# Kernel optimization log

Measured on AMD Instinct MI355X. Metric: run time of the kernel, lower is better.

Reference implementation:

```python
import jax, jax.numpy as jnp
import numpy as np

N_HEADS = 16
SEG_LEN = 512
MSG_LEN = 1536
T_TOTAL = SEG_LEN + MSG_LEN  # 2048


def _build_mask(T):
    # rows < SEG_LEN: attend to all cols < SEG_LEN (full, non-causal block)
    # rows >= SEG_LEN: standard causal (cols <= row)
    rows = jnp.arange(T)[:, None]
    cols = jnp.arange(T)[None, :]
    mask = jnp.where(rows < SEG_LEN, cols < SEG_LEN, cols <= rows)
    return mask  # [T, T] bool


def setup_inputs() -> dict:
    key = jax.random.key(0)
    k1, k2, k3 = jax.random.split(key, 3)
    B, T, E = 4, T_TOTAL, 1024
    x = jax.random.normal(k1, (B, T, E), dtype=jnp.float32)
    W_qkv = jax.random.normal(k2, (E, 3 * E), dtype=jnp.float32) * (1.0 / np.sqrt(E))
    b_qkv = jnp.zeros((3 * E,), dtype=jnp.float32)
    W_proj = jax.random.normal(k3, (E, E), dtype=jnp.float32) * (1.0 / np.sqrt(E))
    b_proj = jnp.zeros((E,), dtype=jnp.float32)
    return {"x": x, "W_qkv": W_qkv, "b_qkv": b_qkv, "W_proj": W_proj, "b_proj": b_proj}


def reference(x, W_qkv, b_qkv, W_proj, b_proj):
    B, T, E = x.shape
    H = N_HEADS
    D = E // H
    qkv = x @ W_qkv + b_qkv  # [B, T, 3E]
    q, k, v = jnp.split(qkv, 3, axis=-1)
    # [B, H, T, D]
    q = q.reshape(B, T, H, D).transpose(0, 2, 1, 3)
    k = k.reshape(B, T, H, D).transpose(0, 2, 1, 3)
    v = v.reshape(B, T, H, D).transpose(0, 2, 1, 3)
    att = jnp.einsum("bhqd,bhkd->bhqk", q, k) * (1.0 / np.sqrt(D))
    mask = _build_mask(T)  # [T, T]
    att = jnp.where(mask[None, None], att, jnp.float32(-jnp.inf))
    att = jax.nn.softmax(att, axis=-1)
    y = jnp.einsum("bhqk,bhkd->bhqd", att, v)
    y = y.transpose(0, 2, 1, 3).reshape(B, T, E)
    return y @ W_proj + b_proj
```

## Files before the change

### kernel.cpp

```cpp
#include <hip/hip_runtime.h>


typedef _Float16 f16;
typedef _Float16 f16x4 __attribute__((ext_vector_type(4)));
typedef _Float16 f16x8 __attribute__((ext_vector_type(8)));
typedef float f32x4 __attribute__((ext_vector_type(4)));

#define MFMA16x32(a, b, c) __builtin_amdgcn_mfma_f32_16x16x32_f16(a, b, c, 0, 0, 0)
#define MFMA16x16(a, b, c) __builtin_amdgcn_mfma_f32_16x16x16f16(a, b, c, 0, 0, 0)

__device__ __forceinline__ void gload_lds16(const void* g, void* l) {
  __builtin_amdgcn_global_load_lds(
      (__attribute__((address_space(1))) void*)g,
      (__attribute__((address_space(3))) void*)l, 16, 0, 0);
}


__global__ void k_cast_f16(const float* __restrict__ x, f16* __restrict__ xh) {
  int i = blockIdx.x * 256 + threadIdx.x;
  float4 v = ((const float4*)x)[i];
  f16x4 o = {(f16)v.x, (f16)v.y, (f16)v.z, (f16)v.w};
  ((f16x4*)xh)[i] = o;
}

__global__ void k_transpose(const float* __restrict__ W, f16* __restrict__ Wt,
                            int Kdim, int Ndim) {
  __shared__ float tile[32][33];
  int n = blockIdx.x * 32 + threadIdx.x;
  int k0 = blockIdx.y * 32;
  for (int j = threadIdx.y; j < 32; j += 8)
    tile[j][threadIdx.x] = W[(size_t)(k0 + j) * Ndim + n];
  __syncthreads();
  int k = k0 + threadIdx.x;
  for (int j = threadIdx.y; j < 32; j += 8)
    Wt[(size_t)(blockIdx.x * 32 + j) * Kdim + k] = (f16)tile[threadIdx.x][j];
}


__global__ __launch_bounds__(256) void k_gemm_qkv(
    const f16* __restrict__ A, const f16* __restrict__ Bt,
    const float* __restrict__ bias,
    f16* __restrict__ Qo, f16* __restrict__ Ko, f16* __restrict__ Vo) {
  constexpr int KD = 1024;
  __shared__ __align__(16) f16 As[128 * 32];
  __shared__ __align__(16) f16 Bs[128 * 32];
  __shared__ __align__(16) f16 Esh[4 * 64 * 72];
  const int tid = threadIdx.x;
  const int wave = tid >> 6, lane = tid & 63;
  const int g = lane >> 4, l16 = lane & 15;
  const int m0 = blockIdx.y * 128, n0 = blockIdx.x * 128;
  const int wm = (wave >> 1) * 64, wn = (wave & 1) * 64;
  const int srow = wave * 16 + (lane >> 2);
  const int skc = (lane & 3) * 8;

  f32x4 acc[4][4] = {};

  for (int k0 = 0; k0 < KD; k0 += 32) {
    __syncthreads();
    for (int it = 0; it < 2; ++it) {
      gload_lds16(A + (size_t)(m0 + it * 64 + srow) * KD + k0 + skc,
                  As + (it * 64 + wave * 16) * 32);
      gload_lds16(Bt + (size_t)(n0 + it * 64 + srow) * KD + k0 + skc,
                  Bs + (it * 64 + wave * 16) * 32);
    }
    __syncthreads();
    f16x8 af[4], bf[4];
    for (int mi = 0; mi < 4; ++mi)
      af[mi] = *(const f16x8*)(As + (wm + mi * 16 + l16) * 32 + g * 8);
    for (int ni = 0; ni < 4; ++ni)
      bf[ni] = *(const f16x8*)(Bs + (wn + ni * 16 + l16) * 32 + g * 8);
    for (int mi = 0; mi < 4; ++mi)
      for (int ni = 0; ni < 4; ++ni)
        acc[mi][ni] = MFMA16x32(af[mi], bf[ni], acc[mi][ni]);
  }

  const int nsub = n0 + wn;
  const int part = nsub >> 10;
  const int h    = (nsub >> 6) & 15;
  const int mg   = m0 + wm;
  const int b    = mg >> 11;
  const int tb   = mg & 2047;
  const size_t bh = (size_t)(b * 16 + h);
  f16* Es = Esh + wave * (64 * 72);

  float bv[4];
  for (int ni = 0; ni < 4; ++ni) bv[ni] = bias[nsub + ni * 16 + l16];

  for (int mi = 0; mi < 4; ++mi)
    for (int ni = 0; ni < 4; ++ni)
      for (int r = 0; r < 4; ++r) {
        f16 hv = (f16)(acc[mi][ni][r] + bv[ni]);
        int mrow = mi * 16 + g * 4 + r, ncol = ni * 16 + l16;
        if (part == 2) Es[ncol * 72 + mrow] = hv;
        else           Es[mrow * 72 + ncol] = hv;
      }

  const int rrow = lane >> 3, rcol = (lane & 7) * 8;
  for (int p = 0; p < 8; ++p) {
    int row = p * 8 + rrow;
    f16x8 vv = *(const f16x8*)(Es + row * 72 + rcol);
    if (part == 0)
      *(f16x8*)(Qo + (bh * 2048 + tb + row) * 64 + rcol) = vv;
    else if (part == 1)
      *(f16x8*)(Ko + (bh * 2048 + tb + row) * 64 + rcol) = vv;
    else
      *(f16x8*)(Vo + (bh * 64 + row) * 2048 + tb + rcol) = vv;
  }
}


__constant__ unsigned char cQA[10] = {15, 14, 13, 12, 11, 10, 9, 8, 7, 5};
__constant__ unsigned char cQB[10] = {255, 255, 255, 255, 0, 1, 2, 3, 6, 4};

__global__ __launch_bounds__(256, 4) void k_attn(
    const f16* __restrict__ Q, const f16* __restrict__ Kb,
    const f16* __restrict__ Vt, f16* __restrict__ Y) {
  __shared__ __align__(16) f16 Ks[64 * 64];
  __shared__ __align__(16) f16 Vs[64 * 64];
  __shared__ __align__(16) f16 Es[4 * 32 * 72];
  __shared__ float rs[4 * 32];

  const int tid = threadIdx.x;
  const int wave = tid >> 6, lane = tid & 63;
  const int g = lane >> 4, l16 = lane & 15;
  const int bh = blockIdx.y;
  const int b = bh >> 4, h = bh & 15;
  const int srowrel = lane >> 3;
  const int sc = (lane & 7) ^ srowrel;

  const f32x4 sinit = {-8.65617025f, -8.65617025f, -8.65617025f, -8.65617025f};

  for (int pass = 0; pass < 2; ++pass) {
    const int qt = pass ? (int)cQB[blockIdx.x] : (int)cQA[blockIdx.x];
    if (qt == 255) break;
    const int q0 = qt * 128;
    const int nt = (qt < 4) ? 8 : (qt + 1) * 2;

    f16x8 aq[2][2];
    for (int mi = 0; mi < 2; ++mi) {
      const f16* qrow =
          Q + ((size_t)bh * 2048 + q0 + wave * 32 + mi * 16 + l16) * 64 + g * 8;
      aq[mi][0] = *(const f16x8*)(qrow);
      aq[mi][1] = *(const f16x8*)(qrow + 32);
      for (int kb = 0; kb < 2; ++kb)
        aq[mi][kb] = aq[mi][kb] * (f16)0.18033688f;
    }

    f32x4 o[2][4] = {};
    float rsum[2] = {};

    for (int i = 0; i < nt; ++i) {
      const int kt0 = i << 6;
      __syncthreads();
      for (int it = 0; it < 2; ++it) {
        int row = it * 32 + wave * 8 + srowrel;
        gload_lds16(Kb + ((size_t)bh * 2048 + kt0 + row) * 64 + sc * 8,
                    Ks + (it * 32 + wave * 8) * 64);
        gload_lds16(Vt + ((size_t)bh * 64 + row) * 2048 + kt0 + sc * 8,
                    Vs + (it * 32 + wave * 8) * 64);
      }
      __syncthreads();

      f32x4 t[2][4];
      for (int nb = 0; nb < 4; ++nb) {
        int R = nb * 16 + l16, sw = R & 7;
        f16x8 bk0 = *(const f16x8*)(Ks + R * 64 + ((0 + g) ^ sw) * 8);
        f16x8 bk1 = *(const f16x8*)(Ks + R * 64 + ((4 + g) ^ sw) * 8);
        for (int mi = 0; mi < 2; ++mi) {
          f32x4 acc = MFMA16x32(bk0, aq[mi][0], sinit);
          t[mi][nb] = MFMA16x32(bk1, aq[mi][1], acc);
        }
      }

      const bool masked = (q0 >= 512) && (kt0 >= q0);
      f16x4 ap[4][2];
      for (int mi = 0; mi < 2; ++mi) {
        const int mrow = q0 + wave * 32 + mi * 16 + l16;
        for (int nb = 0; nb < 4; ++nb)
          for (int r = 0; r < 4; ++r) {
            float p = __builtin_amdgcn_exp2f(t[mi][nb][r]);
            if (masked && (kt0 + nb * 16 + g * 4 + r > mrow)) p = 0.f;
            rsum[mi] += p;
            ap[nb][mi][r] = (f16)p;
          }
      }

      for (int db = 0; db < 4; ++db)
        for (int nb = 0; nb < 4; ++nb) {
          int R = db * 16 + l16, sw = R & 7;
          int c = nb * 2 + (g >> 1);
          f16x4 bv = *(const f16x4*)(Vs + R * 64 + (c ^ sw) * 8 + (g & 1) * 4);
          for (int mi = 0; mi < 2; ++mi)
            o[mi][db] = MFMA16x16(ap[nb][mi], bv, o[mi][db]);
        }
    }

    for (int mi = 0; mi < 2; ++mi) {
      rsum[mi] += __shfl_xor(rsum[mi], 16, 64);
      rsum[mi] += __shfl_xor(rsum[mi], 32, 64);
    }

    if (g == 0)
      for (int mi = 0; mi < 2; ++mi) rs[wave * 32 + mi * 16 + l16] = rsum[mi];
    float rinv[2][4];
    for (int mi = 0; mi < 2; ++mi)
      for (int r = 0; r < 4; ++r)
        rinv[mi][r] = 1.0f / rs[wave * 32 + mi * 16 + g * 4 + r];

    f16* Ew = Es + wave * (32 * 72);
    for (int mi = 0; mi < 2; ++mi)
      for (int db = 0; db < 4; ++db)
        for (int r = 0; r < 4; ++r)
          Ew[(mi * 16 + g * 4 + r) * 72 + db * 16 + l16] =
              (f16)(o[mi][db][r] * rinv[mi][r]);

    const int rrow = lane >> 3, rcol = (lane & 7) * 8;
    const size_t ybase = (size_t)b * 2048 + q0 + wave * 32;
    for (int p = 0; p < 4; ++p) {
      int row = p * 8 + rrow;
      f16x8 vv = *(const f16x8*)(Ew + row * 72 + rcol);
      *(f16x8*)(Y + (ybase + row) * 1024 + h * 64 + rcol) = vv;
    }
  }
}


__global__ __launch_bounds__(256) void k_gemm_proj(
    const f16* __restrict__ A, const f16* __restrict__ Bt,
    const float* __restrict__ bias, float* __restrict__ out) {
  constexpr int KD = 1024;
  __shared__ __align__(16) f16 As[128 * 32];
  __shared__ __align__(16) f16 Bs[128 * 32];
  const int tid = threadIdx.x;
  const int wave = tid >> 6, lane = tid & 63;
  const int g = lane >> 4, l16 = lane & 15;
  const int m0 = blockIdx.y * 128, n0 = blockIdx.x * 128;
  const int wm = (wave >> 1) * 64, wn = (wave & 1) * 64;
  const int srow = wave * 16 + (lane >> 2);
  const int skc = (lane & 3) * 8;

  f32x4 acc[4][4] = {};

  for (int k0 = 0; k0 < KD; k0 += 32) {
    __syncthreads();
    for (int it = 0; it < 2; ++it) {
      gload_lds16(A + (size_t)(m0 + it * 64 + srow) * KD + k0 + skc,
                  As + (it * 64 + wave * 16) * 32);
      gload_lds16(Bt + (size_t)(n0 + it * 64 + srow) * KD + k0 + skc,
                  Bs + (it * 64 + wave * 16) * 32);
    }
    __syncthreads();
    f16x8 af[4], bf[4];
    for (int mi = 0; mi < 4; ++mi)
      af[mi] = *(const f16x8*)(As + (wm + mi * 16 + l16) * 32 + g * 8);
    for (int ni = 0; ni < 4; ++ni)
      bf[ni] = *(const f16x8*)(Bs + (wn + ni * 16 + l16) * 32 + g * 8);
    for (int mi = 0; mi < 4; ++mi)
      for (int ni = 0; ni < 4; ++ni)
        acc[mi][ni] = MFMA16x32(af[mi], bf[ni], acc[mi][ni]);
  }

  float bv[4];
  for (int ni = 0; ni < 4; ++ni) bv[ni] = bias[n0 + wn + ni * 16 + l16];

  for (int mi = 0; mi < 4; ++mi)
    for (int ni = 0; ni < 4; ++ni)
      for (int r = 0; r < 4; ++r) {
        int m = m0 + wm + mi * 16 + g * 4 + r;
        int n = n0 + wn + ni * 16 + l16;
        out[(size_t)m * 1024 + n] = acc[mi][ni][r] + bv[ni];
      }
}


extern "C" void kernel_launch(void* const* d_in, const int* in_sizes, int n_in,
                              void* d_out, int out_size, void* d_ws,
                              size_t ws_size, hipStream_t stream) {
  const float* x      = (const float*)d_in[0];
  const float* W_qkv  = (const float*)d_in[1];
  const float* b_qkv  = (const float*)d_in[2];
  const float* W_proj = (const float*)d_in[3];
  const float* b_proj = (const float*)d_in[4];
  float* out = (float*)d_out;

  char* ws = (char*)d_ws;
  f16* xh    = (f16*)ws;   ws += (size_t)8192 * 1024 * 2;
  f16* Wqt   = (f16*)ws;   ws += (size_t)3072 * 1024 * 2;
  f16* Wpt   = (f16*)ws;   ws += (size_t)1024 * 1024 * 2;
  f16* Qb    = (f16*)ws;   ws += (size_t)64 * 2048 * 64 * 2;
  f16* Kb    = (f16*)ws;   ws += (size_t)64 * 2048 * 64 * 2;
  f16* Vt    = (f16*)ws;   ws += (size_t)64 * 64 * 2048 * 2;
  f16* Y = xh;

  k_cast_f16<<<8192, 256, 0, stream>>>(x, xh);
  k_transpose<<<dim3(96, 32), dim3(32, 8), 0, stream>>>(W_qkv, Wqt, 1024, 3072);
  k_transpose<<<dim3(32, 32), dim3(32, 8), 0, stream>>>(W_proj, Wpt, 1024, 1024);
  k_gemm_qkv<<<dim3(24, 64), 256, 0, stream>>>(xh, Wqt, b_qkv, Qb, Kb, Vt);
  k_attn<<<dim3(10, 64), 256, 0, stream>>>(Qb, Kb, Vt, Y);
  k_gemm_proj<<<dim3(8, 64), 256, 0, stream>>>(Y, Wpt, b_proj, out);
}
```

Measured before the change: 287.1 us.

## Double-buffer K/V tiles in attention kernel to overlap loads with compute

```diff
diff --git a/kernel.cpp b/kernel.cpp
--- a/kernel.cpp
+++ b/kernel.cpp
@@ -112,11 +112,11 @@
 __constant__ unsigned char cQA[10] = {15, 14, 13, 12, 11, 10, 9, 8, 7, 5};
 __constant__ unsigned char cQB[10] = {255, 255, 255, 255, 0, 1, 2, 3, 6, 4};
 
-__global__ __launch_bounds__(256, 4) void k_attn(
+__global__ __launch_bounds__(256, 3) void k_attn(
     const f16* __restrict__ Q, const f16* __restrict__ Kb,
     const f16* __restrict__ Vt, f16* __restrict__ Y) {
-  __shared__ __align__(16) f16 Ks[64 * 64];
-  __shared__ __align__(16) f16 Vs[64 * 64];
+  __shared__ __align__(16) f16 Ks[2][64 * 64];
+  __shared__ __align__(16) f16 Vs[2][64 * 64];
   __shared__ __align__(16) f16 Es[4 * 32 * 72];
   __shared__ float rs[4 * 32];
 
@@ -127,6 +127,7 @@
   const int b = bh >> 4, h = bh & 15;
   const int srowrel = lane >> 3;
   const int sc = (lane & 7) ^ srowrel;
+  const int srw = wave * 8 + srowrel;
 
   const f32x4 sinit = {-8.65617025f, -8.65617025f, -8.65617025f, -8.65617025f};
 
@@ -149,23 +150,37 @@
     f32x4 o[2][4] = {};
     float rsum[2] = {};
 
+    for (int it = 0; it < 2; ++it) {
+      int row = it * 32 + srw;
+      gload_lds16(Kb + ((size_t)bh * 2048 + row) * 64 + sc * 8,
+                  &Ks[0][(it * 32 + wave * 8) * 64]);
+      gload_lds16(Vt + ((size_t)bh * 64 + row) * 2048 + sc * 8,
+                  &Vs[0][(it * 32 + wave * 8) * 64]);
+    }
+    __syncthreads();
+
+    int cur = 0;
     for (int i = 0; i < nt; ++i) {
+      if (i + 1 < nt) {
+        const int kn0 = (i + 1) << 6;
+        for (int it = 0; it < 2; ++it) {
+          int row = it * 32 + srw;
+          gload_lds16(Kb + ((size_t)bh * 2048 + kn0 + row) * 64 + sc * 8,
+                      &Ks[cur ^ 1][(it * 32 + wave * 8) * 64]);
+          gload_lds16(Vt + ((size_t)bh * 64 + row) * 2048 + kn0 + sc * 8,
+                      &Vs[cur ^ 1][(it * 32 + wave * 8) * 64]);
+        }
+      }
+
       const int kt0 = i << 6;
-      __syncthreads();
-      for (int it = 0; it < 2; ++it) {
-        int row = it * 32 + wave * 8 + srowrel;
-        gload_lds16(Kb + ((size_t)bh * 2048 + kt0 + row) * 64 + sc * 8,
-                    Ks + (it * 32 + wave * 8) * 64);
-        gload_lds16(Vt + ((size_t)bh * 64 + row) * 2048 + kt0 + sc * 8,
-                    Vs + (it * 32 + wave * 8) * 64);
-      }
-      __syncthreads();
+      const f16* Kc = Ks[cur];
+      const f16* Vc = Vs[cur];
 
       f32x4 t[2][4];
       for (int nb = 0; nb < 4; ++nb) {
         int R = nb * 16 + l16, sw = R & 7;
-        f16x8 bk0 = *(const f16x8*)(Ks + R * 64 + ((0 + g) ^ sw) * 8);
-        f16x8 bk1 = *(const f16x8*)(Ks + R * 64 + ((4 + g) ^ sw) * 8);
+        f16x8 bk0 = *(const f16x8*)(Kc + R * 64 + ((0 + g) ^ sw) * 8);
+        f16x8 bk1 = *(const f16x8*)(Kc + R * 64 + ((4 + g) ^ sw) * 8);
         for (int mi = 0; mi < 2; ++mi) {
           f32x4 acc = MFMA16x32(bk0, aq[mi][0], sinit);
           t[mi][nb] = MFMA16x32(bk1, aq[mi][1], acc);
@@ -189,10 +204,13 @@
         for (int nb = 0; nb < 4; ++nb) {
           int R = db * 16 + l16, sw = R & 7;
           int c = nb * 2 + (g >> 1);
-          f16x4 bv = *(const f16x4*)(Vs + R * 64 + (c ^ sw) * 8 + (g & 1) * 4);
+          f16x4 bv = *(const f16x4*)(Vc + R * 64 + (c ^ sw) * 8 + (g & 1) * 4);
           for (int mi = 0; mi < 2; ++mi)
             o[mi][db] = MFMA16x16(ap[nb][mi], bv, o[mi][db]);
         }
+
+      __syncthreads();
+      cur ^= 1;
     }
 
     for (int mi = 0; mi < 2; ++mi) {
```

Result: faster. 279.4 us (-2.7%).
